# Optimization experiments

Hardware: AMD Instinct MI355X
Metric: run time of the kernel (lower is better)

## Reference

```python
import jax, jax.numpy as jnp
import numpy as np

B, N, D_IN, D_OUT, H, ALPHA = 8, 2048, 128, 64, 1, 0.2


def setup_inputs() -> dict:
    key = jax.random.key(0)
    k1, k2, k3, k4 = jax.random.split(key, 4)
    x = jax.random.normal(k1, (B, N, D_IN), dtype=jnp.float32)
    adj = jax.random.randint(k2, (B, N, N), 0, 2, dtype=jnp.int32)
    # guarantee self-loops so no softmax row is entirely masked
    adj = jnp.maximum(adj, jnp.eye(N, dtype=jnp.int32)[None])
    # xavier_uniform with gain=1.414, as in the torch module
    lim_w = 1.414 * np.sqrt(6.0 / (D_IN + D_OUT * H))
    W = jax.random.uniform(k3, (D_OUT * H, D_IN), minval=-lim_w, maxval=lim_w, dtype=jnp.float32)
    b = jnp.zeros((D_OUT * H,), dtype=jnp.float32)
    lim_a = 1.414 * np.sqrt(6.0 / (H + 2 * D_OUT))
    a = jax.random.uniform(k4, (H, 2 * D_OUT), minval=-lim_a, maxval=lim_a, dtype=jnp.float32)
    return {"x": x, "adj_hat": adj, "W": W, "b": b, "a": a}


def reference(x, adj_hat, W, b, a):
    Bn, Nn = x.shape[:2]
    # projection: [B,N,d_in] -> [B,N,H,D]
    xp = (x @ W.T + b).reshape(Bn, Nn, H, D_OUT)
    # additive score a . [x_i ; x_j] split into two O(N) dot-products
    # (mathematically identical to the original O(N^2) concat formulation)
    a_src, a_dst = a[:, :D_OUT], a[:, D_OUT:]
    e_src = jnp.einsum('bnhd,hd->bnh', xp, a_src)  # score contribution of node i (query/p axis)
    e_dst = jnp.einsum('bnhd,hd->bnh', xp, a_dst)  # score contribution of node j (neighbor/q axis)
    e = e_src[:, :, None, :] + e_dst[:, None, :, :]  # [B,N,N,H]
    e = jax.nn.leaky_relu(e, ALPHA)
    e = jnp.where(adj_hat[..., None] == 0, -jnp.inf, e)
    att = jax.nn.softmax(e, axis=2)  # softmax over neighbor axis (torch dim=-2)
    res = jnp.einsum('bmnh,bnhd->bmhd', att, xp)  # weighted aggregation
    return res.reshape(Bn, Nn, H * D_OUT)  # concat_heads=True
```

## Files before the change

kernel.cpp:

```cpp
#include <hip/hip_runtime.h>
#include <hip/hip_bf16.h>
#include <cstdint>

#define NN 2048
#define BB 8
#define DIN 128
#define DOUT 64

typedef __attribute__((ext_vector_type(8))) short bf16x8;
typedef __attribute__((ext_vector_type(4))) float f32x4;

static __device__ __forceinline__ unsigned short f2b(float f) {
    union { __hip_bfloat16 h; unsigned short s; } u;
    u.h = __float2bfloat16(f);
    return u.s;
}

__global__ __launch_bounds__(256) void gat_xp_mfma(
    const float* __restrict__ x, const float* __restrict__ W,
    const float* __restrict__ bias, const float* __restrict__ a,
    unsigned short* __restrict__ xpF, float* __restrict__ e_src,
    float* __restrict__ e_dst)
{
    __shared__ float red[4 * 32 * 65];
    const int t = threadIdx.x;
    const int lane = t & 63;
    const int w = t >> 6;
    const int lr = lane & 15;
    const int g  = lane >> 4;
    const int r0 = blockIdx.x * 32;
    const int k0 = w * 32 + g * 8;

    bf16x8 bfr[4];
    #pragma unroll
    for (int dt = 0; dt < 4; ++dt) {
        const float* wr = W + (size_t)(dt * 16 + lr) * DIN + k0;
        const float4 wa = *(const float4*)wr;
        const float4 wb = *(const float4*)(wr + 4);
        bfr[dt][0]=f2b(wa.x); bfr[dt][1]=f2b(wa.y); bfr[dt][2]=f2b(wa.z); bfr[dt][3]=f2b(wa.w);
        bfr[dt][4]=f2b(wb.x); bfr[dt][5]=f2b(wb.y); bfr[dt][6]=f2b(wb.z); bfr[dt][7]=f2b(wb.w);
    }
    #pragma unroll
    for (int half = 0; half < 2; ++half) {
        const float* xr = x + (size_t)(r0 + half * 16 + lr) * DIN + k0;
        const float4 xa = *(const float4*)xr;
        const float4 xb4 = *(const float4*)(xr + 4);
        bf16x8 afr;
        afr[0]=f2b(xa.x);  afr[1]=f2b(xa.y);  afr[2]=f2b(xa.z);  afr[3]=f2b(xa.w);
        afr[4]=f2b(xb4.x); afr[5]=f2b(xb4.y); afr[6]=f2b(xb4.z); afr[7]=f2b(xb4.w);
        #pragma unroll
        for (int dt = 0; dt < 4; ++dt) {
            f32x4 acc = {0.f, 0.f, 0.f, 0.f};
            acc = __builtin_amdgcn_mfma_f32_16x16x32_bf16(afr, bfr[dt], acc, 0, 0, 0);
            #pragma unroll
            for (int reg = 0; reg < 4; ++reg)
                red[w * 2080 + (half * 16 + g * 4 + reg) * 65 + dt * 16 + lr] = acc[reg];
        }
    }
    __syncthreads();

    const int b  = r0 >> 11;
    const int kb = (r0 & (NN - 1)) >> 5;

    #pragma unroll
    for (int i = 0; i < 2; ++i) {
        const int row = i * 16 + (t >> 4);
        const int dq  = t & 15;
        float es = 0.f, ed = 0.f;
        #pragma unroll
        for (int j = 0; j < 4; ++j) {
            const int d = dq * 4 + j;
            const float v = red[0 * 2080 + row * 65 + d] + red[1 * 2080 + row * 65 + d]
                          + red[2 * 2080 + row * 65 + d] + red[3 * 2080 + row * 65 + d]
                          + bias[d];
            es += v * a[d];
            ed += v * a[DOUT + d];
        }
        es += __shfl_xor(es, 1); es += __shfl_xor(es, 2);
        es += __shfl_xor(es, 4); es += __shfl_xor(es, 8);
        ed += __shfl_xor(ed, 1); ed += __shfl_xor(ed, 2);
        ed += __shfl_xor(ed, 4); ed += __shfl_xor(ed, 8);
        if (dq == 0) {
            e_src[r0 + row] = es;
            e_dst[r0 + row] = ed;
        }
    }

    {
        const int dt = w;
        const int d  = dt * 16 + lr;
        const float bv = bias[d];
        bf16x8 frag;
        #pragma unroll
        for (int j = 0; j < 8; ++j) {
            const int row = g * 8 + j;
            const float v = red[0 * 2080 + row * 65 + d] + red[1 * 2080 + row * 65 + d]
                          + red[2 * 2080 + row * 65 + d] + red[3 * 2080 + row * 65 + d]
                          + bv;
            frag[j] = f2b(v);
        }
        *(bf16x8*)(xpF + ((size_t)((b * 4 + dt) * 64 + kb) << 9) + lane * 8) = frag;
    }
}

__global__ __launch_bounds__(256) void gat_attn_mfma(
    const int* __restrict__ adj, const unsigned short* __restrict__ xpF,
    const float* __restrict__ e_src, const float* __restrict__ e_dst,
    float* __restrict__ out)
{
    __shared__ float d_lds[NN];
    __shared__ unsigned int mk[16 * 65];
    __shared__ float mred[4];
    __shared__ float s_lds[16];
    __shared__ float bnd_lds[16];

    const int t = threadIdx.x;
    const int lane = t & 63;
    const int w = t >> 6;
    const int lr = lane & 15;
    const int g  = lane >> 4;
    const int b  = blockIdx.x >> 7;
    const int m0 = (blockIdx.x & 127) * 16;
    const size_t base = (size_t)b * NN;

    const int* __restrict__ arow = adj + ((base + m0) << 11);
    #pragma unroll 4
    for (int s = 0; s < 32; ++s) {
        const int f = s * 1024 + t * 4;
        const int4 v = *(const int4*)(arow + f);
        unsigned int wv = ((v.x != 0) ? 1u : 0u) | ((v.y != 0) ? 2u : 0u)
                        | ((v.z != 0) ? 4u : 0u) | ((v.w != 0) ? 8u : 0u);
        wv <<= ((t & 7) * 4);
        wv |= __shfl_xor(wv, 1);
        wv |= __shfl_xor(wv, 2);
        wv |= __shfl_xor(wv, 4);
        if ((t & 7) == 0)
            mk[(f >> 11) * 65 + ((f & (NN - 1)) >> 5)] = wv;
    }

    float dm = -1e30f;
    #pragma unroll
    for (int i = 0; i < 8; ++i) {
        const float v = e_dst[base + i * 256 + t];
        d_lds[i * 256 + t] = v;
        dm = fmaxf(dm, v);
    }
    #pragma unroll
    for (int off = 32; off >= 1; off >>= 1) dm = fmaxf(dm, __shfl_xor(dm, off));
    if (lane == 0) mred[w] = dm;
    __syncthreads();
    const float dmax = fmaxf(fmaxf(mred[0], mred[1]), fmaxf(mred[2], mred[3]));
    if (t < 16) {
        const float s = e_src[base + m0 + t];
        const float e0 = s + dmax;
        s_lds[t] = s;
        bnd_lds[t] = fmaxf(e0, 0.2f * e0);
    }
    __syncthreads();

    const float sreg = s_lds[lr];
    const float bnd  = bnd_lds[lr];

    f32x4 acc = {0.f, 0.f, 0.f, 0.f};
    float rs = 0.f;
    const unsigned short* __restrict__ xv =
        xpF + ((size_t)((b * 4 + w) * 64) << 9) + lane * 8;

    #pragma unroll 8
    for (int ks = 0; ks < 64; ++ks) {
        const unsigned int mw = mk[lr * 65 + ks];
        const float4 d0 = *(const float4*)(d_lds + ks * 32 + g * 8);
        const float4 d1 = *(const float4*)(d_lds + ks * 32 + g * 8 + 4);
        const float dvv[8] = {d0.x, d0.y, d0.z, d0.w, d1.x, d1.y, d1.z, d1.w};
        bf16x8 afr;
        #pragma unroll
        for (int j = 0; j < 8; ++j) {
            const float e = sreg + dvv[j];
            const float le = fmaxf(e, 0.2f * e);
            const float pe = __expf(le - bnd);
            const float p = ((mw >> (g * 8 + j)) & 1u) ? pe : 0.f;
            rs += p;
            afr[j] = f2b(p);
        }
        const bf16x8 bfr = *(const bf16x8*)(xv + (size_t)ks * 512);
        acc = __builtin_amdgcn_mfma_f32_16x16x32_bf16(afr, bfr, acc, 0, 0, 0);
    }

    rs += __shfl_xor(rs, 16);
    rs += __shfl_xor(rs, 32);

    #pragma unroll
    for (int reg = 0; reg < 4; ++reg) {
        const int row = g * 4 + reg;
        const float nrm = __shfl(rs, row);
        out[(base + (size_t)(m0 + row)) * DOUT + w * 16 + lr] = acc[reg] / nrm;
    }
}

extern "C" void kernel_launch(void* const* d_in, const int* in_sizes, int n_in,
                              void* d_out, int out_size, void* d_ws, size_t ws_size,
                              hipStream_t stream) {
    const float* x    = (const float*)d_in[0];
    const int*   adj  = (const int*)d_in[1];
    const float* W    = (const float*)d_in[2];
    const float* bvec = (const float*)d_in[3];
    const float* a    = (const float*)d_in[4];
    float* out = (float*)d_out;

    unsigned short* xpF = (unsigned short*)d_ws;
    float* e_src = (float*)((char*)d_ws + (1 << 21));
    float* e_dst = e_src + (size_t)BB * NN;

    gat_xp_mfma<<<(BB * NN) / 32, 256, 0, stream>>>(x, W, bvec, a, xpF, e_src, e_dst);
    gat_attn_mfma<<<BB * (NN / 16), 256, 0, stream>>>(adj, xpF, e_src, e_dst, out);
}
```

Before: 253.8 us.

## Split attention k-range across waves to avoid redundant exp computation

```diff
diff --git a/kernel.cpp b/kernel.cpp
--- a/kernel.cpp
+++ b/kernel.cpp
@@ -110,6 +110,8 @@
 {
     __shared__ float d_lds[NN];
     __shared__ unsigned int mk[16 * 65];
+    __shared__ float red[4][4][16][17];
+    __shared__ float rs_lds[4 * 16];
     __shared__ float mred[4];
     __shared__ float s_lds[16];
     __shared__ float bnd_lds[16];
@@ -161,16 +163,17 @@
     const float sreg = s_lds[lr];
     const float bnd  = bnd_lds[lr];
 
-    f32x4 acc = {0.f, 0.f, 0.f, 0.f};
+    f32x4 acc[4] = {};
     float rs = 0.f;
-    const unsigned short* __restrict__ xv =
-        xpF + ((size_t)((b * 4 + w) * 64) << 9) + lane * 8;
-
-    #pragma unroll 8
-    for (int ks = 0; ks < 64; ++ks) {
-        const unsigned int mw = mk[lr * 65 + ks];
-        const float4 d0 = *(const float4*)(d_lds + ks * 32 + g * 8);
-        const float4 d1 = *(const float4*)(d_lds + ks * 32 + g * 8 + 4);
+    const unsigned short* __restrict__ xbase = xpF + ((size_t)(b * 4) << 15);
+    const int kk0 = w * 16;
+
+    #pragma unroll 4
+    for (int ks = 0; ks < 16; ++ks) {
+        const int kk = kk0 + ks;
+        const unsigned int mw = mk[lr * 65 + kk];
+        const float4 d0 = *(const float4*)(d_lds + kk * 32 + g * 8);
+        const float4 d1 = *(const float4*)(d_lds + kk * 32 + g * 8 + 4);
         const float dvv[8] = {d0.x, d0.y, d0.z, d0.w, d1.x, d1.y, d1.z, d1.w};
         bf16x8 afr;
         #pragma unroll
@@ -182,18 +185,34 @@
             rs += p;
             afr[j] = f2b(p);
         }
-        const bf16x8 bfr = *(const bf16x8*)(xv + (size_t)ks * 512);
-        acc = __builtin_amdgcn_mfma_f32_16x16x32_bf16(afr, bfr, acc, 0, 0, 0);
+        #pragma unroll
+        for (int dt = 0; dt < 4; ++dt) {
+            const bf16x8 bfr =
+                *(const bf16x8*)(xbase + ((size_t)(dt * 64 + kk) << 9) + lane * 8);
+            acc[dt] = __builtin_amdgcn_mfma_f32_16x16x32_bf16(afr, bfr, acc[dt], 0, 0, 0);
+        }
     }
 
     rs += __shfl_xor(rs, 16);
     rs += __shfl_xor(rs, 32);
-
-    #pragma unroll
-    for (int reg = 0; reg < 4; ++reg) {
-        const int row = g * 4 + reg;
-        const float nrm = __shfl(rs, row);
-        out[(base + (size_t)(m0 + row)) * DOUT + w * 16 + lr] = acc[reg] / nrm;
+    if (lane < 16) rs_lds[w * 16 + lane] = rs;
+
+    #pragma unroll
+    for (int dt = 0; dt < 4; ++dt)
+        #pragma unroll
+        for (int reg = 0; reg < 4; ++reg)
+            red[w][dt][g * 4 + reg][lr] = acc[dt][reg];
+    __syncthreads();
+
+    const int row = t >> 4;
+    const int col = t & 15;
+    const float nrm = 1.f / (rs_lds[row] + rs_lds[16 + row]
+                           + rs_lds[32 + row] + rs_lds[48 + row]);
+    #pragma unroll
+    for (int dt = 0; dt < 4; ++dt) {
+        const float v = red[0][dt][row][col] + red[1][dt][row][col]
+                      + red[2][dt][row][col] + red[3][dt][row][col];
+        out[(base + (size_t)(m0 + row)) * DOUT + dt * 16 + col] = v * nrm;
     }
 }
 
```

New measurement: 225.2 us. -11.3%, faster.
